# Kernel tuning notes

Measured on AMD Instinct MI355X. Metric: run time of the kernel, lower is better.

Reference implementation:

```python
import jax, jax.numpy as jnp
import numpy as np

CS = 64          # chunk_size
CP = CS - 1      # causal_padding
H = 8            # heads
DH = 64          # dim_head
SCALE = DH ** -0.5


def rotate_half(x):
    x1, x2 = jnp.split(x, 2, axis=-1)
    return jnp.concatenate((-x2, x1), axis=-1)


def apply_rope(t, freqs):
    rd = freqs.shape[-1]
    t_rot, t_pass = t[..., :rd], t[..., rd:]
    t_rot = t_rot * jnp.cos(freqs) + rotate_half(t_rot) * jnp.sin(freqs)
    return jnp.concatenate((t_rot, t_pass), axis=-1)


def setup_inputs() -> dict:
    key = jax.random.key(0)
    ks = jax.random.split(key, 10)
    b, n, dim = 4, 4096, 1024
    k_chunks, r, rlen = 64, 2, 128
    inner = H * DH
    return {
        "x": jax.random.normal(ks[0], (b, n, dim), dtype=jnp.float32),
        "context": jax.random.normal(ks[1], (b, k_chunks, r, rlen, dim), dtype=jnp.float32),
        "q_pos_emb": jax.random.normal(ks[2], (1, 1, CS, DH), dtype=jnp.float32),
        "k_pos_emb": jax.random.normal(ks[3], (1, 1, rlen, DH), dtype=jnp.float32),
        "Wq": jax.random.normal(ks[4], (dim, inner), dtype=jnp.float32) * 0.02,
        "Wk": jax.random.normal(ks[5], (dim, inner), dtype=jnp.float32) * 0.02,
        "Wv": jax.random.normal(ks[6], (dim, inner), dtype=jnp.float32) * 0.02,
        "Wo": jax.random.normal(ks[7], (inner, dim), dtype=jnp.float32) * 0.02,
        "bo": jnp.zeros((dim,), dtype=jnp.float32),
        "null_k": jax.random.normal(ks[8], (inner,), dtype=jnp.float32),
        "null_v": jax.random.normal(ks[9], (inner,), dtype=jnp.float32),
    }


def reference(x, context, q_pos_emb, k_pos_emb, Wq, Wk, Wv, Wo, bo, null_k, null_v):
    b, n, dim = x.shape
    _, k_chunks, r, rlen, _ = context.shape
    # causal shift: drop first CP tokens, pad CP zeros at end (F.pad with -CP)
    xs = jnp.pad(x[:, CP:], ((0, 0), (0, CP), (0, 0)))
    seq_index = (n // CS) * CS
    rem = n - seq_index
    xs = xs[:, :seq_index]                                   # [b, k*CS, dim]
    # shift q rope the same way; pad region gets freqs=0 -> identity rotation
    qpe = jnp.pad(q_pos_emb[:, :, CP:], ((0, 0), (0, 0), (0, CP), (0, 0)))
    kpe = jnp.tile(k_pos_emb, (1, 1, r, 1))                  # [1,1,r*rlen,DH]
    bk = b * k_chunks
    xc = xs.reshape(bk, CS, dim)
    ctx = context.reshape(bk, r * rlen, dim)
    # projections -> [bk, h, seq, dh]
    q = (xc @ Wq).reshape(bk, CS, H, DH).transpose(0, 2, 1, 3) * SCALE
    k = (ctx @ Wk).reshape(bk, r * rlen, H, DH).transpose(0, 2, 1, 3)
    v = (ctx @ Wv).reshape(bk, r * rlen, H, DH).transpose(0, 2, 1, 3)
    q = apply_rope(q, qpe)
    k = apply_rope(k, kpe)
    # null kv prepend
    nk = jnp.broadcast_to(null_k.reshape(1, H, 1, DH), (bk, H, 1, DH))
    nv = jnp.broadcast_to(null_v.reshape(1, H, 1, DH), (bk, H, 1, DH))
    k = jnp.concatenate((nk, k), axis=2)
    v = jnp.concatenate((nv, v), axis=2)
    sim = jnp.einsum('bhid,bhjd->bhij', q, k)
    attn = jax.nn.softmax(sim, axis=-1)
    o = jnp.einsum('bhij,bhjd->bhid', attn, v)
    o = o.transpose(0, 2, 1, 3).reshape(bk, CS, H * DH)
    o = o @ Wo + bo                                          # [bk, CS, dim]
    o = o.reshape(b, k_chunks * CS, dim)
    # unshift: pad CP zeros at front, trim CP - rem from end
    o = jnp.concatenate(
        (jnp.zeros((b, CP, dim), o.dtype), o[:, :k_chunks * CS - CP + rem]), axis=1)
    return o
```

## Files before the change

kernel.cpp:

```cpp
#include <hip/hip_runtime.h>


#define DEV __device__ __forceinline__

typedef __bf16 bf16x8 __attribute__((ext_vector_type(8)));
typedef float f32x4 __attribute__((ext_vector_type(4)));

DEV unsigned short f2bf(float f) {
  union { float f; unsigned int u; } v; v.f = f;
  unsigned int u = v.u;
  unsigned int r = (u + 0x7FFFu + ((u >> 16) & 1u)) >> 16;
  return (unsigned short)r;
}
DEV float bf2f(unsigned short h) {
  union { unsigned int u; float f; } v; v.u = ((unsigned int)h) << 16;
  return v.f;
}
DEV float bfelem(bf16x8 v, int i) {
  union { bf16x8 v; unsigned short u[8]; } t; t.v = v;
  return bf2f(t.u[i]);
}
DEV unsigned int pkbf(unsigned int hi, unsigned int lo) {
  return __builtin_amdgcn_perm(hi, lo, 0x07060302u);
}
DEV unsigned int pk2(float lo, float hi) {
  return ((unsigned int)f2bf(hi) << 16) | f2bf(lo);
}

DEV void ldst16(const void* g, void* l) {
  __builtin_amdgcn_global_load_lds(
      (const __attribute__((address_space(1))) void*)g,
      (__attribute__((address_space(3))) void*)l, 16, 0, 0);
}

DEV void bar() { __builtin_amdgcn_s_barrier(); }
#define VMCNT4 asm volatile("s_waitcnt vmcnt(4)" ::: "memory")
#define VMCNT0 asm volatile("s_waitcnt vmcnt(0)" ::: "memory")

__global__ __launch_bounds__(256) void prep_k(const float* __restrict__ Wq,
                                              const float* __restrict__ Wk,
                                              const float* __restrict__ Wv,
                                              const float* __restrict__ Wo,
                                              const float* __restrict__ qpe,
                                              const float* __restrict__ kpe,
                                              unsigned short* __restrict__ Wqt,
                                              unsigned short* __restrict__ Wkt,
                                              unsigned short* __restrict__ Wvt,
                                              unsigned short* __restrict__ Wot,
                                              float* __restrict__ ck, float* __restrict__ sk,
                                              float* __restrict__ cq, float* __restrict__ sq,
                                              float* __restrict__ out) {
  __shared__ float tl[64][65];
  int blk = blockIdx.x;
  int tid = threadIdx.x;
  if (blk < 512) {
    int mat = blk >> 7, loc = blk & 127;
    const float* W;
    unsigned short* Wt;
    int R, C;
    float scale = 1.0f;
    if (mat == 0)      { W = Wq; Wt = Wqt; R = 1024; C = 512; scale = 0.125f; }
    else if (mat == 1) { W = Wk; Wt = Wkt; R = 1024; C = 512; }
    else if (mat == 2) { W = Wv; Wt = Wvt; R = 1024; C = 512; }
    else               { W = Wo; Wt = Wot; R = 512;  C = 1024; }
    int nct = C >> 6;
    int rt = loc / nct, ct = loc % nct;
    int r0 = rt << 6, c0 = ct << 6;
    #pragma unroll
    for (int i = 0; i < 16; ++i) {
      int flat = i * 256 + tid;
      int rr = flat >> 6, cc = flat & 63;
      tl[rr][cc] = W[(size_t)(r0 + rr) * C + c0 + cc] * scale;
    }
    __syncthreads();
    #pragma unroll
    for (int i = 0; i < 16; ++i) {
      int flat = i * 256 + tid;
      int cc = flat >> 6, rr = flat & 63;
      Wt[(size_t)(c0 + cc) * R + r0 + rr] = f2bf(tl[rr][cc]);
    }
  } else if (blk < 764) {
    int r = blk - 512;
    int b = r / 63, rr = r % 63;
    float4 z = {0.f, 0.f, 0.f, 0.f};
    *(float4*)(out + (((size_t)(b * 4096 + rr)) << 10) + tid * 4) = z;
  } else {
    int t = (blk - 764) * 256 + tid;
    float f = kpe[t];
    ck[t] = cosf(f);
    sk[t] = sinf(f);
    if (t < 64) {
      float g = qpe[63 * 64 + t];
      cq[t] = cosf(g);
      sq[t] = sinf(g);
    }
  }
}

__global__ __launch_bounds__(256) void cast_all(const float* __restrict__ ctx,
                                                const float* __restrict__ x,
                                                unsigned short* __restrict__ ctxb,
                                                unsigned short* __restrict__ xb) {
  int id = blockIdx.x;
  if (id < 32768) {
    size_t base = ((size_t)id * 256 + threadIdx.x) * 8;
    uint4 lo = *(const uint4*)(ctx + base);
    uint4 hi = *(const uint4*)(ctx + base + 4);
    uint4 pk;
    pk.x = pkbf(lo.y, lo.x);
    pk.y = pkbf(lo.w, lo.z);
    pk.z = pkbf(hi.y, hi.x);
    pk.w = pkbf(hi.w, hi.z);
    *(uint4*)(ctxb + base) = pk;
  } else {
    size_t e = ((size_t)(id - 32768) * 256 + threadIdx.x) * 8;
    int m = (int)(e >> 10), c = (int)(e & 1023);
    int b = m >> 12, t = m & 4095;
    uint4 pk = {0, 0, 0, 0};
    if (t <= 4032) {
      const float* s = x + (((size_t)(b << 12) + t + 63) << 10) + c;
      uint4 lo = *(const uint4*)s;
      uint4 hi = *(const uint4*)(s + 4);
      pk.x = pkbf(lo.y, lo.x);
      pk.y = pkbf(lo.w, lo.z);
      pk.z = pkbf(hi.y, hi.x);
      pk.w = pkbf(hi.w, hi.z);
    }
    *(uint4*)(xb + e) = pk;
  }
}

DEV bf16x8 rdfrag(const unsigned short* b, int row, int c) {
  return *(const bf16x8*)((const char*)b + row * 128 + ((c ^ (row & 7)) << 4));
}
DEV bf16x8 rdfrag512(const unsigned short* b, int row, int c) {
  return *(const bf16x8*)((const char*)b + row * 512 + ((c ^ (row & 7)) << 4));
}

DEV void rdA(const unsigned short* bufA, int wm, int ln15, int l4, int mtb,
             bf16x8 (&af)[2][2]) {
  #pragma unroll
  for (int mq = 0; mq < 2; ++mq)
    #pragma unroll
    for (int kk = 0; kk < 2; ++kk)
      af[mq][kk] = rdfrag(bufA, wm + (mtb + mq) * 16 + ln15, kk * 4 + l4);
}

DEV void rdB(const unsigned short* bufB, int wn, int ln15, int l4, bf16x8 (&bf)[4][2]) {
  #pragma unroll
  for (int nt = 0; nt < 4; ++nt)
    #pragma unroll
    for (int kk = 0; kk < 2; ++kk)
      bf[nt][kk] = rdfrag(bufB, wn + nt * 16 + ln15, kk * 4 + l4);
}

template <int MTB>
DEV void mfma16(const bf16x8 (&af)[2][2], const bf16x8 (&bf)[4][2], f32x4 (&acc)[8][4]) {
  __builtin_amdgcn_s_setprio(1);
  #pragma unroll
  for (int mq = 0; mq < 2; ++mq)
    #pragma unroll
    for (int nt = 0; nt < 4; ++nt)
      #pragma unroll
      for (int kk = 0; kk < 2; ++kk)
        acc[MTB + mq][nt] = __builtin_amdgcn_mfma_f32_16x16x32_bf16(
            af[mq][kk], bf[nt][kk], acc[MTB + mq][nt], 0, 0, 0);
  __builtin_amdgcn_s_setprio(0);
}

DEV void stgF(unsigned short* buf, const unsigned short* src, int r0, int w,
              int Lrow, int srcC, int k0, int ldK) {
  #pragma unroll
  for (int q = 0; q < 4; ++q) {
    ldst16(src + (size_t)(r0 + q * 64 + w * 8 + Lrow) * ldK + (k0 + srcC * 8),
           (char*)buf + ((q * 512 + w * 64) << 4));
  }
}

template <int KD>
DEV void kloopP(const unsigned short* __restrict__ A, const unsigned short* __restrict__ B,
                unsigned short* sh, f32x4 (&acc)[8][4], int m0, int n0, int tid) {
  unsigned short* Abase = sh;
  unsigned short* Bbase = sh + 49152;
  int w = tid >> 6, lane = tid & 63;
  int wm = (w & 1) * 128, wn = (w >> 1) * 64;
  int ln15 = lane & 15, l4 = lane >> 4;
  int Lrow = lane >> 3;
  int srcC = (lane & 7) ^ (Lrow & 7);
  const int MSK = KD - 1;
  const int NT = KD / 64;

  stgF(Abase,         A, m0, w, Lrow, srcC, 0, KD);
  stgF(Bbase,         B, n0, w, Lrow, srcC, 0, KD);
  stgF(Abase + 16384, A, m0, w, Lrow, srcC, 64, KD);
  VMCNT4;
  bar();

  for (int t = 0; t < NT; ++t) {
    const int k0 = t * 64;
    unsigned short* Ar = Abase + (t % 3) * 16384;
    unsigned short* As = Abase + ((t + 2) % 3) * 16384;
    unsigned short* Br = Bbase + (t & 1) * 16384;
    unsigned short* Bs = Bbase + ((t + 1) & 1) * 16384;
    bf16x8 af[2][2], bf[4][2];

    rdB(Br, wn, ln15, l4, bf);
    rdA(Ar, wm, ln15, l4, 0, af);
    stgF(Bs, B, n0, w, Lrow, srcC, (k0 + 64) & MSK, KD);
    bar(); mfma16<0>(af, bf, acc); bar();

    rdA(Ar, wm, ln15, l4, 2, af);
    bar(); mfma16<2>(af, bf, acc); bar();

    rdA(Ar, wm, ln15, l4, 4, af);
    stgF(As, A, m0, w, Lrow, srcC, (k0 + 128) & MSK, KD);
    bar(); mfma16<4>(af, bf, acc); bar();

    rdA(Ar, wm, ln15, l4, 6, af);
    VMCNT4;
    bar(); mfma16<6>(af, bf, acc); bar();
  }

  VMCNT0;
  bar();
}

__global__ __launch_bounds__(512, 2) void proj8(const unsigned short* __restrict__ ctxb,
                                                const unsigned short* __restrict__ xb,
                                                const unsigned short* __restrict__ Wkt,
                                                const unsigned short* __restrict__ Wvt,
                                                const unsigned short* __restrict__ Wqt,
                                                unsigned short* __restrict__ kb,
                                                unsigned short* __restrict__ vtg,
                                                unsigned short* __restrict__ qbuf,
                                                const float* __restrict__ ck,
                                                const float* __restrict__ sk,
                                                const float* __restrict__ cq,
                                                const float* __restrict__ sq) {
  __shared__ unsigned short sh[81920];
  int id = blockIdx.x;
  int mode, m0, n0;
  const unsigned short *A, *B;
  if (id < 1024) {
    int x = (id & 7) + 8 * (id >> 5);
    int j = (id >> 3) & 3;
    int y = j & 1, z = j >> 1;
    mode = z;
    A = ctxb; B = z ? Wvt : Wkt;
    m0 = x << 8; n0 = y << 8;
  } else {
    int t = id - 1024;
    int x = (t & 7) + 8 * (t >> 4);
    int y = (t >> 3) & 1;
    mode = 2;
    A = xb; B = Wqt;
    m0 = x << 8; n0 = y << 8;
  }
  int tid = threadIdx.x, w = tid >> 6, lane = tid & 63;
  int wm = (w & 1) * 128, wn = (w >> 1) * 64;
  int ln15 = lane & 15, l4 = lane >> 4;

  f32x4 acc[8][4] = {};
  kloopP<1024>(A, B, sh, acc, m0, n0, tid);

  if (mode == 0) {
    #pragma unroll
    for (int mt = 0; mt < 8; ++mt)
      #pragma unroll
      for (int r = 0; r < 4; ++r) {
        int m = m0 + wm + mt * 16 + l4 * 4 + r;
        int fib = (m & 127) << 6;
        #pragma unroll
        for (int nt = 0; nt < 4; ++nt) {
          int d = nt * 16 + ln15;
          float partner = acc[mt][nt ^ 2][r];
          float val = acc[mt][nt][r] * ck[fib + d] + (nt < 2 ? -partner : partner) * sk[fib + d];
          kb[(size_t)m * 512 + n0 + wn + d] = f2bf(val);
        }
      }
  } else if (mode == 1) {
    #pragma unroll
    for (int mt = 0; mt < 8; ++mt)
      #pragma unroll
      for (int nt = 0; nt < 4; ++nt)
        #pragma unroll
        for (int r = 0; r < 4; ++r) {
          int ml = wm + mt * 16 + l4 * 4 + r;
          int nl = wn + nt * 16 + ln15;
          int mc = ml >> 3, me = ml & 7;
          *(unsigned short*)((char*)sh + nl * 512 + ((mc ^ (nl & 31)) << 4) + me * 2) =
              f2bf(acc[mt][nt][r]);
        }
    __syncthreads();
    #pragma unroll
    for (int i = 0; i < 16; ++i) {
      int flat = i * 512 + tid;
      int nl = flat >> 5, mc = flat & 31;
      uint4 v = *(const uint4*)((const char*)sh + nl * 512 + ((mc ^ (nl & 31)) << 4));
      *(uint4*)(vtg + (size_t)(n0 + nl) * 65536 + m0 + mc * 8) = v;
    }
  } else {
    #pragma unroll
    for (int mt = 0; mt < 8; ++mt)
      #pragma unroll
      for (int nt = 0; nt < 4; ++nt)
        #pragma unroll
        for (int r = 0; r < 4; ++r) {
          int m = m0 + wm + mt * 16 + l4 * 4 + r;
          int n = n0 + wn + nt * 16 + ln15;
          float val = acc[mt][nt][r];
          if ((m & 63) == 0) {
            int d = nt * 16 + ln15;
            float partner = acc[mt][nt ^ 2][r];
            val = val * cq[d] + (nt < 2 ? -partner : partner) * sq[d];
          }
          qbuf[(size_t)m * 512 + n] = f2bf(val);
        }
  }
}

__global__ __launch_bounds__(512, 2) void out8(const unsigned short* __restrict__ A,
                                               const unsigned short* __restrict__ B,
                                               const float* __restrict__ bias,
                                               float* __restrict__ out) {
  __shared__ unsigned short sh[81920];
  int id = blockIdx.x;
  int x = (id & 7) + 8 * (id >> 5);
  int y = (id >> 3) & 3;
  int m0 = x << 8, n0 = y << 8;
  int tid = threadIdx.x, w = tid >> 6, lane = tid & 63;
  int wm = (w & 1) * 128, wn = (w >> 1) * 64;
  int ln15 = lane & 15, l4 = lane >> 4;

  f32x4 acc[8][4] = {};
  kloopP<512>(A, B, sh, acc, m0, n0, tid);

  #pragma unroll
  for (int mt = 0; mt < 8; ++mt)
    #pragma unroll
    for (int nt = 0; nt < 4; ++nt)
      #pragma unroll
      for (int r = 0; r < 4; ++r) {
        int m = m0 + wm + mt * 16 + l4 * 4 + r;
        int n = n0 + wn + nt * 16 + ln15;
        int b = m >> 12, t = m & 4095;
        if (t <= 4032)
          out[((size_t)((b << 12) + t + 63)) * 1024 + n] = acc[mt][nt][r] + bias[n];
      }
}

__global__ __launch_bounds__(256) void attn_kernel(const unsigned short* __restrict__ qb,
                                                   const unsigned short* __restrict__ kb,
                                                   const unsigned short* __restrict__ vtg,
                                                   const float* __restrict__ nullk,
                                                   const float* __restrict__ nullv,
                                                   unsigned short* __restrict__ ob) {
  __shared__ unsigned short qs[64 * 64];
  __shared__ unsigned short ks[256 * 64];
  __shared__ unsigned short vs[64 * 256];
  int id = blockIdx.x;
  int bc = (id & 7) + 8 * (id >> 6);
  int h = (id >> 3) & 7;
  int tid = threadIdx.x, w = tid >> 6, lane = tid & 63;
  int ln15 = lane & 15, l4 = lane >> 4;
  int Lrow = lane >> 3, srcC = (lane & 7) ^ (Lrow & 7);

  #pragma unroll
  for (int q8 = 0; q8 < 2; ++q8) {
    int t = w * 2 + q8;
    ldst16(qb + (size_t)(bc * 64 + t * 8 + Lrow) * 512 + h * 64 + srcC * 8, (char*)qs + t * 1024);
  }
  #pragma unroll
  for (int q8 = 0; q8 < 8; ++q8) {
    int t = w * 8 + q8;
    ldst16(kb + (size_t)(bc * 256 + t * 8 + Lrow) * 512 + h * 64 + srcC * 8, (char*)ks + t * 1024);
  }
  #pragma unroll
  for (int q8 = 0; q8 < 8; ++q8) {
    int t = w * 8 + q8;
    int dd = t * 2 + (lane >> 5);
    int cl = (lane & 31) ^ (dd & 7);
    ldst16(vtg + (size_t)(h * 64 + dd) * 65536 + bc * 256 + cl * 8, (char*)vs + t * 1024);
  }
  __syncthreads();

  int q = w * 16 + ln15;

  float ns = 0.f;
  {
    bf16x8 q0 = rdfrag(qs, q, l4 * 2);
    bf16x8 q1 = rdfrag(qs, q, l4 * 2 + 1);
    const float* nkp = nullk + h * 64 + l4 * 16;
    #pragma unroll
    for (int i = 0; i < 8; ++i) ns += bfelem(q0, i) * nkp[i];
    #pragma unroll
    for (int i = 0; i < 8; ++i) ns += bfelem(q1, i) * nkp[8 + i];
    ns += __shfl_xor(ns, 16);
    ns += __shfl_xor(ns, 32);
  }
  float rnull = __expf(ns);

  f32x4 acc[16] = {};
  #pragma unroll
  for (int k32 = 0; k32 < 2; ++k32) {
    int c = k32 * 4 + l4;
    bf16x8 bq = rdfrag(qs, q, c);
    #pragma unroll
    for (int nt = 0; nt < 16; ++nt) {
      bf16x8 ak = rdfrag(ks, nt * 16 + ln15, c);
      acc[nt] = __builtin_amdgcn_mfma_f32_16x16x32_bf16(ak, bq, acc[nt], 0, 0, 0);
    }
  }

  float s = 0.f;
  #pragma unroll
  for (int nt = 0; nt < 16; ++nt)
    #pragma unroll
    for (int r = 0; r < 4; ++r) {
      float p = __expf(acc[nt][r]);
      acc[nt][r] = p;
      s += p;
    }
  s += __shfl_xor(s, 16);
  s += __shfl_xor(s, 32);
  float rsum = s + rnull;

  __syncthreads();

  #pragma unroll
  for (int nt = 0; nt < 16; ++nt) {
    unsigned int w0 = pk2(acc[nt][0], acc[nt][1]);
    unsigned int w1 = pk2(acc[nt][2], acc[nt][3]);
    int j = nt * 16 + l4 * 4;
    int cj = j >> 3;
    int off = (j & 7) * 2;
    uint2 v = {w0, w1};
    *(uint2*)((char*)ks + q * 512 + ((cj ^ (q & 7)) << 4) + off) = v;
  }
  f32x4 oacc[4] = {};
  #pragma unroll
  for (int kk = 0; kk < 8; ++kk) {
    int c = kk * 4 + l4;
    bf16x8 bp = rdfrag512(ks, q, c);
    #pragma unroll
    for (int nt = 0; nt < 4; ++nt) {
      bf16x8 av = rdfrag512(vs, nt * 16 + ln15, c);
      oacc[nt] = __builtin_amdgcn_mfma_f32_16x16x32_bf16(av, bp, oacc[nt], 0, 0, 0);
    }
  }

  float inv = 1.0f / rsum;
  #pragma unroll
  for (int nt = 0; nt < 4; ++nt) {
    const float* nvp = nullv + h * 64 + nt * 16 + l4 * 4;
    float4 nv4 = *(const float4*)nvp;
    float o0 = (oacc[nt][0] + rnull * nv4.x) * inv;
    float o1 = (oacc[nt][1] + rnull * nv4.y) * inv;
    float o2 = (oacc[nt][2] + rnull * nv4.z) * inv;
    float o3 = (oacc[nt][3] + rnull * nv4.w) * inv;
    uint2 v = {pk2(o0, o1), pk2(o2, o3)};
    *(uint2*)(ob + ((size_t)(bc * 64 + q) * 8 + h) * 64 + nt * 16 + l4 * 4) = v;
  }
}

extern "C" void kernel_launch(void* const* d_in, const int* in_sizes, int n_in,
                              void* d_out, int out_size, void* d_ws, size_t ws_size,
                              hipStream_t stream) {
  const float* x = (const float*)d_in[0];
  const float* ctx = (const float*)d_in[1];
  const float* qpe = (const float*)d_in[2];
  const float* kpe = (const float*)d_in[3];
  const float* Wq = (const float*)d_in[4];
  const float* Wk = (const float*)d_in[5];
  const float* Wv = (const float*)d_in[6];
  const float* Wo = (const float*)d_in[7];
  const float* bo = (const float*)d_in[8];
  const float* nk = (const float*)d_in[9];
  const float* nv = (const float*)d_in[10];
  float* out = (float*)d_out;
  char* ws = (char*)d_ws;

  unsigned short* Wqt  = (unsigned short*)(ws + 0);
  unsigned short* Wkt  = (unsigned short*)(ws + 1048576);
  unsigned short* Wvt  = (unsigned short*)(ws + 2097152);
  unsigned short* Wot  = (unsigned short*)(ws + 3145728);
  float* cosk = (float*)(ws + 4194304);
  float* sink = (float*)(ws + 4227072);
  float* cosq = (float*)(ws + 4259840);
  float* sinq = (float*)(ws + 4260096);
  unsigned short* qb   = (unsigned short*)(ws + 8388608);
  unsigned short* kb   = (unsigned short*)(ws + 25165824);
  unsigned short* vtg  = (unsigned short*)(ws + 92274688);
  unsigned short* obuf = (unsigned short*)(ws + 159383552);
  unsigned short* xb   = (unsigned short*)(ws + 176160768);
  unsigned short* ctxb = (unsigned short*)(ws + 209715200);

  prep_k<<<796, 256, 0, stream>>>(Wq, Wk, Wv, Wo, qpe, kpe, Wqt, Wkt, Wvt, Wot,
                                  cosk, sink, cosq, sinq, out);

  cast_all<<<40960, 256, 0, stream>>>(ctx, x, ctxb, xb);

  proj8<<<1152, 512, 0, stream>>>(ctxb, xb, Wkt, Wvt, Wqt, kb, vtg, qb,
                                  cosk, sink, cosq, sinq);

  attn_kernel<<<2048, 256, 0, stream>>>(qb, kb, vtg, nk, nv, obuf);

  out8<<<256, 512, 0, stream>>>(obuf, Wot, bo, out);
}
```

Measured before the change: 688.9 us.

## Replace pipelined 256x256 GEMM tiles with simple 128x128 single-buffered tiles

```diff
diff --git a/kernel.cpp b/kernel.cpp
--- a/kernel.cpp
+++ b/kernel.cpp
@@ -32,10 +32,6 @@
       (const __attribute__((address_space(1))) void*)g,
       (__attribute__((address_space(3))) void*)l, 16, 0, 0);
 }
-
-DEV void bar() { __builtin_amdgcn_s_barrier(); }
-#define VMCNT4 asm volatile("s_waitcnt vmcnt(4)" ::: "memory")
-#define VMCNT0 asm volatile("s_waitcnt vmcnt(0)" ::: "memory")
 
 __global__ __launch_bounds__(256) void prep_k(const float* __restrict__ Wq,
                                               const float* __restrict__ Wk,
@@ -137,150 +133,101 @@
   return *(const bf16x8*)((const char*)b + row * 512 + ((c ^ (row & 7)) << 4));
 }
 
-DEV void rdA(const unsigned short* bufA, int wm, int ln15, int l4, int mtb,
-             bf16x8 (&af)[2][2]) {
-  #pragma unroll
-  for (int mq = 0; mq < 2; ++mq)
-    #pragma unroll
-    for (int kk = 0; kk < 2; ++kk)
-      af[mq][kk] = rdfrag(bufA, wm + (mtb + mq) * 16 + ln15, kk * 4 + l4);
-}
-
-DEV void rdB(const unsigned short* bufB, int wn, int ln15, int l4, bf16x8 (&bf)[4][2]) {
-  #pragma unroll
-  for (int nt = 0; nt < 4; ++nt)
-    #pragma unroll
-    for (int kk = 0; kk < 2; ++kk)
-      bf[nt][kk] = rdfrag(bufB, wn + nt * 16 + ln15, kk * 4 + l4);
-}
-
-template <int MTB>
-DEV void mfma16(const bf16x8 (&af)[2][2], const bf16x8 (&bf)[4][2], f32x4 (&acc)[8][4]) {
-  __builtin_amdgcn_s_setprio(1);
-  #pragma unroll
-  for (int mq = 0; mq < 2; ++mq)
-    #pragma unroll
-    for (int nt = 0; nt < 4; ++nt)
-      #pragma unroll
-      for (int kk = 0; kk < 2; ++kk)
-        acc[MTB + mq][nt] = __builtin_amdgcn_mfma_f32_16x16x32_bf16(
-            af[mq][kk], bf[nt][kk], acc[MTB + mq][nt], 0, 0, 0);
-  __builtin_amdgcn_s_setprio(0);
-}
-
-DEV void stgF(unsigned short* buf, const unsigned short* src, int r0, int w,
-              int Lrow, int srcC, int k0, int ldK) {
-  #pragma unroll
-  for (int q = 0; q < 4; ++q) {
-    ldst16(src + (size_t)(r0 + q * 64 + w * 8 + Lrow) * ldK + (k0 + srcC * 8),
-           (char*)buf + ((q * 512 + w * 64) << 4));
-  }
-}
-
 template <int KD>
-DEV void kloopP(const unsigned short* __restrict__ A, const unsigned short* __restrict__ B,
-                unsigned short* sh, f32x4 (&acc)[8][4], int m0, int n0, int tid) {
-  unsigned short* Abase = sh;
-  unsigned short* Bbase = sh + 49152;
+DEV void kloop97(const unsigned short* __restrict__ A, const unsigned short* __restrict__ B,
+                 unsigned short* sh, f32x4 (&acc)[4][4], int m0, int n0, int tid) {
+  unsigned short* As = sh;
+  unsigned short* Bs = sh + 8192;
   int w = tid >> 6, lane = tid & 63;
-  int wm = (w & 1) * 128, wn = (w >> 1) * 64;
-  int ln15 = lane & 15, l4 = lane >> 4;
-  int Lrow = lane >> 3;
-  int srcC = (lane & 7) ^ (Lrow & 7);
-  const int MSK = KD - 1;
-  const int NT = KD / 64;
-
-  stgF(Abase,         A, m0, w, Lrow, srcC, 0, KD);
-  stgF(Bbase,         B, n0, w, Lrow, srcC, 0, KD);
-  stgF(Abase + 16384, A, m0, w, Lrow, srcC, 64, KD);
-  VMCNT4;
-  bar();
-
-  for (int t = 0; t < NT; ++t) {
-    const int k0 = t * 64;
-    unsigned short* Ar = Abase + (t % 3) * 16384;
-    unsigned short* As = Abase + ((t + 2) % 3) * 16384;
-    unsigned short* Br = Bbase + (t & 1) * 16384;
-    unsigned short* Bs = Bbase + ((t + 1) & 1) * 16384;
-    bf16x8 af[2][2], bf[4][2];
-
-    rdB(Br, wn, ln15, l4, bf);
-    rdA(Ar, wm, ln15, l4, 0, af);
-    stgF(Bs, B, n0, w, Lrow, srcC, (k0 + 64) & MSK, KD);
-    bar(); mfma16<0>(af, bf, acc); bar();
-
-    rdA(Ar, wm, ln15, l4, 2, af);
-    bar(); mfma16<2>(af, bf, acc); bar();
-
-    rdA(Ar, wm, ln15, l4, 4, af);
-    stgF(As, A, m0, w, Lrow, srcC, (k0 + 128) & MSK, KD);
-    bar(); mfma16<4>(af, bf, acc); bar();
-
-    rdA(Ar, wm, ln15, l4, 6, af);
-    VMCNT4;
-    bar(); mfma16<6>(af, bf, acc); bar();
-  }
-
-  VMCNT0;
-  bar();
-}
-
-__global__ __launch_bounds__(512, 2) void proj8(const unsigned short* __restrict__ ctxb,
-                                                const unsigned short* __restrict__ xb,
-                                                const unsigned short* __restrict__ Wkt,
-                                                const unsigned short* __restrict__ Wvt,
-                                                const unsigned short* __restrict__ Wqt,
-                                                unsigned short* __restrict__ kb,
-                                                unsigned short* __restrict__ vtg,
-                                                unsigned short* __restrict__ qbuf,
-                                                const float* __restrict__ ck,
-                                                const float* __restrict__ sk,
-                                                const float* __restrict__ cq,
-                                                const float* __restrict__ sq) {
-  __shared__ unsigned short sh[81920];
+  int wm = (w & 1) * 64, wn = (w >> 1) * 64;
+  int Lrow = lane >> 3, Lc = lane & 7;
+  int srcC = Lc ^ (Lrow & 7);
+
+  for (int k0 = 0; k0 < KD; k0 += 64) {
+    #pragma unroll
+    for (int q = 0; q < 4; ++q) {
+      int t = w * 4 + q;
+      ldst16(A + (size_t)(m0 + t * 8 + Lrow) * KD + (k0 + srcC * 8), (char*)As + t * 1024);
+      ldst16(B + (size_t)(n0 + t * 8 + Lrow) * KD + (k0 + srcC * 8), (char*)Bs + t * 1024);
+    }
+    __syncthreads();
+    #pragma unroll
+    for (int k32 = 0; k32 < 2; ++k32) {
+      int c = k32 * 4 + (lane >> 4);
+      bf16x8 af[4], bfr[4];
+      #pragma unroll
+      for (int mt = 0; mt < 4; ++mt)
+        af[mt] = rdfrag(As, wm + mt * 16 + (lane & 15), c);
+      #pragma unroll
+      for (int nt = 0; nt < 4; ++nt)
+        bfr[nt] = rdfrag(Bs, wn + nt * 16 + (lane & 15), c);
+      #pragma unroll
+      for (int mt = 0; mt < 4; ++mt)
+        #pragma unroll
+        for (int nt = 0; nt < 4; ++nt)
+          acc[mt][nt] = __builtin_amdgcn_mfma_f32_16x16x32_bf16(af[mt], bfr[nt], acc[mt][nt], 0, 0, 0);
+    }
+    __syncthreads();
+  }
+}
+
+__global__ __launch_bounds__(256) void proj97(const unsigned short* __restrict__ ctxb,
+                                              const unsigned short* __restrict__ xb,
+                                              const unsigned short* __restrict__ Wkt,
+                                              const unsigned short* __restrict__ Wvt,
+                                              const unsigned short* __restrict__ Wqt,
+                                              unsigned short* __restrict__ kb,
+                                              unsigned short* __restrict__ vtg,
+                                              unsigned short* __restrict__ qbuf,
+                                              const float* __restrict__ ck,
+                                              const float* __restrict__ sk,
+                                              const float* __restrict__ cq,
+                                              const float* __restrict__ sq) {
+  __shared__ unsigned short sh[16384];
   int id = blockIdx.x;
   int mode, m0, n0;
   const unsigned short *A, *B;
-  if (id < 1024) {
-    int x = (id & 7) + 8 * (id >> 5);
-    int j = (id >> 3) & 3;
-    int y = j & 1, z = j >> 1;
+  if (id < 4096) {
+    int x = (id & 7) + 8 * (id >> 6);
+    int j = (id >> 3) & 7;
+    int y = j & 3, z = j >> 2;
     mode = z;
     A = ctxb; B = z ? Wvt : Wkt;
-    m0 = x << 8; n0 = y << 8;
+    m0 = x * 128; n0 = y * 128;
   } else {
-    int t = id - 1024;
-    int x = (t & 7) + 8 * (t >> 4);
-    int y = (t >> 3) & 1;
+    int t = id - 4096;
+    int x = (t & 7) + 8 * (t >> 5);
+    int y = (t >> 3) & 3;
     mode = 2;
     A = xb; B = Wqt;
-    m0 = x << 8; n0 = y << 8;
+    m0 = x * 128; n0 = y * 128;
   }
   int tid = threadIdx.x, w = tid >> 6, lane = tid & 63;
-  int wm = (w & 1) * 128, wn = (w >> 1) * 64;
+  int wm = (w & 1) * 64, wn = (w >> 1) * 64;
   int ln15 = lane & 15, l4 = lane >> 4;
 
-  f32x4 acc[8][4] = {};
-  kloopP<1024>(A, B, sh, acc, m0, n0, tid);
+  f32x4 acc[4][4] = {};
+  kloop97<1024>(A, B, sh, acc, m0, n0, tid);
 
   if (mode == 0) {
     #pragma unroll
-    for (int mt = 0; mt < 8; ++mt)
+    for (int mt = 0; mt < 4; ++mt)
       #pragma unroll
       for (int r = 0; r < 4; ++r) {
         int m = m0 + wm + mt * 16 + l4 * 4 + r;
         int fib = (m & 127) << 6;
         #pragma unroll
         for (int nt = 0; nt < 4; ++nt) {
+          int n = n0 + wn + nt * 16 + ln15;
           int d = nt * 16 + ln15;
           float partner = acc[mt][nt ^ 2][r];
           float val = acc[mt][nt][r] * ck[fib + d] + (nt < 2 ? -partner : partner) * sk[fib + d];
-          kb[(size_t)m * 512 + n0 + wn + d] = f2bf(val);
+          kb[(size_t)m * 512 + n] = f2bf(val);
         }
       }
   } else if (mode == 1) {
     #pragma unroll
-    for (int mt = 0; mt < 8; ++mt)
+    for (int mt = 0; mt < 4; ++mt)
       #pragma unroll
       for (int nt = 0; nt < 4; ++nt)
         #pragma unroll
@@ -288,20 +235,20 @@
           int ml = wm + mt * 16 + l4 * 4 + r;
           int nl = wn + nt * 16 + ln15;
           int mc = ml >> 3, me = ml & 7;
-          *(unsigned short*)((char*)sh + nl * 512 + ((mc ^ (nl & 31)) << 4) + me * 2) =
+          *(unsigned short*)((char*)sh + nl * 256 + ((mc ^ (nl & 15)) * 16) + me * 2) =
               f2bf(acc[mt][nt][r]);
         }
     __syncthreads();
     #pragma unroll
-    for (int i = 0; i < 16; ++i) {
-      int flat = i * 512 + tid;
-      int nl = flat >> 5, mc = flat & 31;
-      uint4 v = *(const uint4*)((const char*)sh + nl * 512 + ((mc ^ (nl & 31)) << 4));
+    for (int i = 0; i < 8; ++i) {
+      int flat = i * 256 + tid;
+      int nl = flat >> 4, mc = flat & 15;
+      uint4 v = *(const uint4*)((const char*)sh + nl * 256 + ((mc ^ (nl & 15)) * 16));
       *(uint4*)(vtg + (size_t)(n0 + nl) * 65536 + m0 + mc * 8) = v;
     }
   } else {
     #pragma unroll
-    for (int mt = 0; mt < 8; ++mt)
+    for (int mt = 0; mt < 4; ++mt)
       #pragma unroll
       for (int nt = 0; nt < 4; ++nt)
         #pragma unroll
@@ -319,24 +266,23 @@
   }
 }
 
-__global__ __launch_bounds__(512, 2) void out8(const unsigned short* __restrict__ A,
-                                               const unsigned short* __restrict__ B,
-                                               const float* __restrict__ bias,
-                                               float* __restrict__ out) {
-  __shared__ unsigned short sh[81920];
+__global__ __launch_bounds__(256) void out97(const unsigned short* __restrict__ A,
+                                             const unsigned short* __restrict__ B,
+                                             const float* __restrict__ bias,
+                                             float* __restrict__ out) {
+  __shared__ unsigned short sh[16384];
   int id = blockIdx.x;
-  int x = (id & 7) + 8 * (id >> 5);
-  int y = (id >> 3) & 3;
-  int m0 = x << 8, n0 = y << 8;
+  int x = (id & 7) + 8 * (id >> 6), y = (id >> 3) & 7;
+  int m0 = x * 128, n0 = y * 128;
   int tid = threadIdx.x, w = tid >> 6, lane = tid & 63;
-  int wm = (w & 1) * 128, wn = (w >> 1) * 64;
+  int wm = (w & 1) * 64, wn = (w >> 1) * 64;
   int ln15 = lane & 15, l4 = lane >> 4;
 
-  f32x4 acc[8][4] = {};
-  kloopP<512>(A, B, sh, acc, m0, n0, tid);
-
-  #pragma unroll
-  for (int mt = 0; mt < 8; ++mt)
+  f32x4 acc[4][4] = {};
+  kloop97<512>(A, B, sh, acc, m0, n0, tid);
+
+  #pragma unroll
+  for (int mt = 0; mt < 4; ++mt)
     #pragma unroll
     for (int nt = 0; nt < 4; ++nt)
       #pragma unroll
@@ -500,10 +446,10 @@
 
   cast_all<<<40960, 256, 0, stream>>>(ctx, x, ctxb, xb);
 
-  proj8<<<1152, 512, 0, stream>>>(ctxb, xb, Wkt, Wvt, Wqt, kb, vtg, qb,
-                                  cosk, sink, cosq, sinq);
+  proj97<<<4608, 256, 0, stream>>>(ctxb, xb, Wkt, Wvt, Wqt, kb, vtg, qb,
+                                   cosk, sink, cosq, sinq);
 
   attn_kernel<<<2048, 256, 0, stream>>>(qb, kb, vtg, nk, nv, obuf);
 
-  out8<<<256, 512, 0, stream>>>(obuf, Wot, bo, out);
-}
+  out97<<<1024, 256, 0, stream>>>(obuf, Wot, bo, out);
+}
```

Result: slower. 767.4 us (+11.4%).
